# Kernel optimization log

Measured on AMD Instinct MI355X. Metric: run time of the kernel, lower is better.

## Reference

```python
import jax, jax.numpy as jnp
import numpy as np

DIM = 192; RES = (8, 56, 56); HEADS = 6; WS = (2, 7, 7); SS = (1, 3, 3)
B = 2
N_WIN_TOK = WS[0] * WS[1] * WS[2]  # 98


def _rel_pos_index():
    # 3D Swin relative position index, (N, N) int
    Wd, Wh, Ww = WS
    coords = np.stack(np.meshgrid(np.arange(Wd), np.arange(Wh), np.arange(Ww), indexing='ij'))
    coords = coords.reshape(3, -1)  # (3, N)
    rel = (coords[:, :, None] - coords[:, None, :]).transpose(1, 2, 0)  # (N, N, 3)
    rel[:, :, 0] += Wd - 1
    rel[:, :, 1] += Wh - 1
    rel[:, :, 2] += Ww - 1
    rel[:, :, 0] *= (2 * Wh - 1) * (2 * Ww - 1)
    rel[:, :, 1] *= (2 * Ww - 1)
    return rel.sum(-1)


def _attn_mask():
    # shifted-window mask (nW, N, N), 0 / -100
    D, H, W = RES; Wd, Wh, Ww = WS; sd, sh, sw = SS
    img = np.zeros((D, H, W))
    cnt = 0
    for ds in (slice(0, -Wd), slice(-Wd, -sd), slice(-sd, None)):
        for hs in (slice(0, -Wh), slice(-Wh, -sh), slice(-sh, None)):
            for ws_ in (slice(0, -Ww), slice(-Ww, -sw), slice(-sw, None)):
                img[ds, hs, ws_] = cnt
                cnt += 1
    win = img.reshape(D // Wd, Wd, H // Wh, Wh, W // Ww, Ww)
    win = win.transpose(0, 2, 4, 1, 3, 5).reshape(-1, N_WIN_TOK)  # (nW, N)
    diff = win[:, :, None] - win[:, None, :]
    return np.where(diff != 0, -100.0, 0.0).astype(np.float32)


_REL_IDX = _rel_pos_index()
_MASK = _attn_mask()


def _window_partition(x):
    # (B, D, H, W, C) -> (B*nW, N, C)
    Bb, D, H, W, C = x.shape
    Wd, Wh, Ww = WS
    x = x.reshape(Bb, D // Wd, Wd, H // Wh, Wh, W // Ww, Ww, C)
    x = x.transpose(0, 1, 3, 5, 2, 4, 6, 7)
    return x.reshape(-1, N_WIN_TOK, C)


def _window_reverse(x, Bb):
    # (B*nW, N, C) -> (B, D, H, W, C)
    D, H, W = RES; Wd, Wh, Ww = WS
    C = x.shape[-1]
    x = x.reshape(Bb, D // Wd, H // Wh, W // Ww, Wd, Wh, Ww, C)
    x = x.transpose(0, 1, 4, 2, 5, 3, 6, 7)
    return x.reshape(Bb, D, H, W, C)


def _layernorm(x, g, b, eps=1e-5):
    mu = jnp.mean(x, -1, keepdims=True)
    var = jnp.var(x, -1, keepdims=True)
    return (x - mu) * jax.lax.rsqrt(var + eps) * g + b


def setup_inputs() -> dict:
    key = jax.random.key(0)
    ks = jax.random.split(key, 8)
    L = RES[0] * RES[1] * RES[2]
    s = 0.02
    return {
        'x': jax.random.normal(ks[0], (B, L, DIM), jnp.float32),
        'norm1_g': jnp.ones((DIM,), jnp.float32),
        'norm1_b': jnp.zeros((DIM,), jnp.float32),
        'qkv_w': jax.random.normal(ks[1], (3 * DIM, DIM), jnp.float32) * s,
        'qkv_b': jax.random.normal(ks[2], (3 * DIM,), jnp.float32) * s,
        'rel_table': jax.random.normal(ks[3], ((2 * WS[0] - 1) * (2 * WS[1] - 1) * (2 * WS[2] - 1), HEADS), jnp.float32) * s,
        'norm2_g': jnp.ones((DIM,), jnp.float32),
        'norm2_b': jnp.zeros((DIM,), jnp.float32),
        'mlp_w1': jax.random.normal(ks[4], (4 * DIM, DIM), jnp.float32) * s,
        'mlp_b1': jax.random.normal(ks[5], (4 * DIM,), jnp.float32) * s,
        'mlp_w2': jax.random.normal(ks[6], (DIM, 4 * DIM), jnp.float32) * s,
        'mlp_b2': jax.random.normal(ks[7], (4 * DIM // 4,), jnp.float32) * s,
    }


def reference(x, norm1_g, norm1_b, qkv_w, qkv_b, rel_table, norm2_g, norm2_b, mlp_w1, mlp_b1, mlp_w2, mlp_b2):
    Bb, L, C = x.shape
    D, H, W = RES
    hd = C // HEADS
    scale = hd ** (-0.5)

    short_cut = x
    xn = _layernorm(x, norm1_g, norm1_b).reshape(Bb, D, H, W, C)
    xs = jnp.roll(xn, (-SS[0], -SS[1], -SS[2]), axis=(1, 2, 3))
    xw = _window_partition(xs)  # (Bn, N, C)
    Bn, N, _ = xw.shape

    # qkv grouping matches original: (nH hD qkv), qkv fastest axis
    qkv = (jnp.einsum('bnc,oc->bno', xw, qkv_w) + qkv_b).reshape(Bn, N, HEADS, hd, 3)
    q = qkv[..., 0].transpose(0, 2, 1, 3)  # (Bn, nH, N, hd)
    k = qkv[..., 1].transpose(0, 2, 1, 3)
    v = qkv[..., 2].transpose(0, 2, 1, 3)

    attn = jnp.einsum('bhnd,bhmd->bhnm', q, k) * scale
    bias = rel_table[jnp.asarray(_REL_IDX.reshape(-1))].reshape(N, N, HEADS)
    attn = attn + bias.transpose(2, 0, 1)[None]  # (Bn, nH, N, N)

    mask = jnp.asarray(_MASK)  # (nW, N, N)
    nW = mask.shape[0]
    attn = attn.reshape(Bb, nW, HEADS, N, N) + mask[None, :, None]
    attn = jax.nn.softmax(attn.reshape(Bn, HEADS, N, N), axis=-1)

    out = jnp.einsum('bhnm,bhmd->bhnd', attn, v)
    out = out.transpose(0, 2, 1, 3).reshape(Bn, N, C)

    xr = _window_reverse(out, Bb)
    x2 = jnp.roll(xr, (SS[0], SS[1], SS[2]), axis=(1, 2, 3)).reshape(Bb, L, C) + short_cut

    short_cut2 = x2
    h = _layernorm(x2, norm2_g, norm2_b)
    h = jax.nn.relu(jnp.einsum('blc,oc->blo', h, mlp_w1) + mlp_b1)
    h = jax.nn.relu(jnp.einsum('blo,co->blc', h, mlp_w2) + mlp_b2)
    return h + short_cut2
```

## Files before the change

### kernel.cpp

```cpp
#include <hip/hip_runtime.h>

typedef unsigned short u16;
typedef unsigned int   u32;
typedef __attribute__((ext_vector_type(4))) float f32x4;
typedef __attribute__((ext_vector_type(8))) short s16x8;
typedef __attribute__((ext_vector_type(4))) u32   u32x4;
typedef __attribute__((ext_vector_type(4))) u16   u16x4;

#define DEV static __device__ __forceinline__

DEV float bf2f(u16 a) { union { u32 u; float f; } x; x.u = ((u32)a) << 16; return x.f; }
DEV u16 f2bf(float f) {
  union { float f; u32 u; } x; x.f = f;
  u32 r = (x.u + 0x7FFFu + ((x.u >> 16) & 1u)) >> 16;
  return (u16)r;
}
DEV float wsum(float v) {
#pragma unroll
  for (int m = 32; m; m >>= 1) v += __shfl_xor(v, m, 64);
  return v;
}

DEV void gload16(const void* g, void* l) {
  __builtin_amdgcn_global_load_lds(
      (const __attribute__((address_space(1))) u32*)g,
      (__attribute__((address_space(3))) u32*)l, 16, 0, 0);
}

DEV const s16x8* frag(const u16* lds, int row, int s) {
  int sw = (s & ~7) | ((s & 7) ^ (row & 7));
  return reinterpret_cast<const s16x8*>(
      reinterpret_cast<const char*>(lds) + row * 384 + sw * 16);
}


__global__ __launch_bounds__(256) void k_prep(
    const float* __restrict__ qkvw, const float* __restrict__ qkvb,
    u16* __restrict__ qkvwb, float* __restrict__ pbias,
    const float* __restrict__ w1, u16* __restrict__ w1b,
    const float* __restrict__ relt, u16* __restrict__ biasT)
{
  int b = blockIdx.x, tid = threadIdx.x;
  if (b < 108) {
    const float sc = 0.17677669529663687f;
    int i = b * 256 + tid;
    if (i < 27648) {
      int np = i / 48, c = i - np * 48;
      int t = np / 192, rem = np - t * 192;
      int head = rem >> 5, dd = rem & 31;
      int o = head * 96 + dd * 3 + t;
      float s2 = (t == 0) ? sc : 1.f;
      f32x4 v = reinterpret_cast<const f32x4*>(qkvw)[o * 48 + c];
      u16x4 ov; ov[0] = f2bf(v[0] * s2); ov[1] = f2bf(v[1] * s2);
      ov[2] = f2bf(v[2] * s2); ov[3] = f2bf(v[3] * s2);
      reinterpret_cast<u16x4*>(qkvwb)[i] = ov;
    }
    if (i < 576) {
      int t = i / 192, rem = i - t * 192;
      int head = rem >> 5, dd = rem & 31;
      pbias[i] = qkvb[head * 96 + dd * 3 + t] * ((t == 0) ? sc : 1.f);
    }
  } else if (b < 252) {
    int i = (b - 108) * 256 + tid;
    if (i < 36864) {
      f32x4 v = reinterpret_cast<const f32x4*>(w1)[i];
      u16x4 o; o[0] = f2bf(v[0]); o[1] = f2bf(v[1]); o[2] = f2bf(v[2]); o[3] = f2bf(v[3]);
      reinterpret_cast<u16x4*>(w1b)[i] = o;
    }
  } else {
    int i = (b - 252) * 256 + tid;
    if (i >= 602112) return;
    int t = i % 112; int rem = i / 112;
    int j = rem % 112; rem /= 112;
    int h = rem % 6; int c = rem / 6;
    if (j >= 98) { biasT[i] = f2bf(-1e30f); return; }
    if (t >= 98) { biasT[i] = 0; return; }
    int td = t >= 49, tr = t - td * 49, th = tr / 7, tw = tr - th * 7;
    int jd = j >= 49, jr = j - jd * 49, jh = jr / 7, jw = jr - jh * 7;
    int lin_t = td * 169 + th * 13 + tw;
    int lin_j = jd * 169 + jh * 13 + jw;
    float bias = relt[(lin_t - lin_j + 253) * 6 + h];
    int cd = (c >> 2) & 1, ch = (c >> 1) & 1, cw = c & 1;
    int cnt_t = (cd ? (1 + td) : 0) * 9 + (ch ? (1 + (th >= 4)) : 0) * 3 + (cw ? (1 + (tw >= 4)) : 0);
    int cnt_j = (cd ? (1 + jd) : 0) * 9 + (ch ? (1 + (jh >= 4)) : 0) * 3 + (cw ? (1 + (jw >= 4)) : 0);
    if (cnt_t != cnt_j) bias -= 100.f;
    biasT[i] = f2bf(bias);
  }
}

__global__ __launch_bounds__(256) void k_wconv(const float* __restrict__ s, u16* __restrict__ d, int n4) {
  int i = blockIdx.x * 256 + threadIdx.x;
  if (i < n4) {
    f32x4 v = reinterpret_cast<const f32x4*>(s)[i];
    u16x4 o; o[0] = f2bf(v[0]); o[1] = f2bf(v[1]); o[2] = f2bf(v[2]); o[3] = f2bf(v[3]);
    reinterpret_cast<u16x4*>(d)[i] = o;
  }
}

__global__ __launch_bounds__(256) void k_ln1_win(
    const float* __restrict__ x, const float* __restrict__ g, const float* __restrict__ b,
    u16* __restrict__ xw)
{
  int row  = blockIdx.x * 4 + (threadIdx.x >> 6);
  int lane = threadIdx.x & 63;
  int win = row / 98, tok = row - win * 98;
  int bb = win >> 8, wrem = win & 255;
  int wd = wrem >> 6, wh = (wrem >> 3) & 7, ww = wrem & 7;
  int td = tok >= 49; int tr = tok - td * 49; int th = tr / 7, tw = tr - th * 7;
  int dsrc = (wd * 2 + td + 1) & 7;
  int hs = wh * 7 + th + 3; if (hs >= 56) hs -= 56;
  int wsc = ww * 7 + tw + 3; if (wsc >= 56) wsc -= 56;
  const float* xr = x + ((size_t)bb * 25088 + (size_t)dsrc * 3136 + hs * 56 + wsc) * 192;
  float v0 = xr[lane], v1 = xr[lane + 64], v2 = xr[lane + 128];
  float mu  = wsum(v0 + v1 + v2) * (1.f / 192.f);
  float sq  = wsum(v0 * v0 + v1 * v1 + v2 * v2) * (1.f / 192.f);
  float inv = rsqrtf(sq - mu * mu + 1e-5f);
  u16* orow = xw + (size_t)row * 192;
  orow[lane      ] = f2bf((v0 - mu) * inv * g[lane      ] + b[lane      ]);
  orow[lane + 64 ] = f2bf((v1 - mu) * inv * g[lane + 64 ] + b[lane + 64 ]);
  orow[lane + 128] = f2bf((v2 - mu) * inv * g[lane + 128] + b[lane + 128]);
}

__global__ __launch_bounds__(256) void k_merge_ln2(
    const float* __restrict__ x, const u16* __restrict__ ao,
    const float* __restrict__ g, const float* __restrict__ b,
    u16* __restrict__ x2b, u16* __restrict__ xn2)
{
  int m = blockIdx.x * 4 + (threadIdx.x >> 6);
  int lane = threadIdx.x & 63;
  int bb = m / 25088, l = m - bb * 25088;
  int d = l / 3136; int rem = l - d * 3136; int h = rem / 56, w = rem - h * 56;
  int dsh = (d + 7) & 7;
  int hsh = h - 3; if (hsh < 0) hsh += 56;
  int wsh = w - 3; if (wsh < 0) wsh += 56;
  int wd = dsh >> 1, td = dsh & 1;
  int wh = hsh / 7, th = hsh - wh * 7;
  int ww = wsh / 7, tw = wsh - ww * 7;
  int win = (bb << 8) + (wd << 6) + (wh << 3) + ww;
  int tok = td * 49 + th * 7 + tw;
  const u16* ar = ao + ((size_t)win * 98 + tok) * 192;
  const float* xr = x + (size_t)m * 192;
  float v0 = xr[lane      ] + bf2f(ar[lane      ]);
  float v1 = xr[lane + 64 ] + bf2f(ar[lane + 64 ]);
  float v2 = xr[lane + 128] + bf2f(ar[lane + 128]);
  u16* x2r = x2b + (size_t)m * 192;
  x2r[lane] = f2bf(v0); x2r[lane + 64] = f2bf(v1); x2r[lane + 128] = f2bf(v2);
  float mu  = wsum(v0 + v1 + v2) * (1.f / 192.f);
  float sq  = wsum(v0 * v0 + v1 * v1 + v2 * v2) * (1.f / 192.f);
  float inv = rsqrtf(sq - mu * mu + 1e-5f);
  u16* nr = xn2 + (size_t)m * 192;
  nr[lane      ] = f2bf((v0 - mu) * inv * g[lane      ] + b[lane      ]);
  nr[lane + 64 ] = f2bf((v1 - mu) * inv * g[lane + 64 ] + b[lane + 64 ]);
  nr[lane + 128] = f2bf((v2 - mu) * inv * g[lane + 128] + b[lane + 128]);
}

template<bool RELU, int NTOT>
__global__ __launch_bounds__(256) void k_gemm3(
    const u16* __restrict__ A, const u16* __restrict__ Wb, const float* __restrict__ bias,
    u16* __restrict__ C)
{
  constexpr int MG = 8;
  __shared__ u16 As[2][64 * 192];
  int bid = blockIdx.x;
  int nb = bid / 98, mg = bid - nb * 98;
  int n0 = nb * 96;
  int m_base = mg * (MG * 64);
  int tid = threadIdx.x, lane = tid & 63, wv = tid >> 6;
  int lr = lane & 15, lg = lane >> 4;
  int wm = wv >> 1, wn = wv & 1;

  auto stage = [&](int buf, int mt) {
    const char* gb = (const char*)(A + (size_t)(m_base + mt * 64) * 192);
    char* lb = (char*)As[buf] + wv * 6144;
#pragma unroll
    for (int c = 0; c < 6144; c += 1024) {
      int o = wv * 6144 + c + lane * 16;
      int row = (int)((u32)o / 384u);
      int slot = (o - row * 384) >> 4;
      int sw = (slot & ~7) | ((slot & 7) ^ (row & 7));
      gload16(gb + (size_t)row * 384 + sw * 16, lb + c);
    }
  };

  stage(0, 0);

  s16x8 wf[3][6];
  const u16* wbase = Wb + (size_t)(n0 + wn * 48 + lr) * 192 + lg * 8;
#pragma unroll
  for (int nf = 0; nf < 3; ++nf)
#pragma unroll
    for (int ks = 0; ks < 6; ++ks)
      wf[nf][ks] = *reinterpret_cast<const s16x8*>(wbase + (size_t)nf * 16 * 192 + ks * 32);
  float bs[3];
#pragma unroll
  for (int nf = 0; nf < 3; ++nf) bs[nf] = bias[n0 + wn * 48 + nf * 16 + lr];

  __syncthreads();
  for (int i = 0; i < MG; ++i) {
    int cur = i & 1;
    if (i + 1 < MG) stage(cur ^ 1, i + 1);
    f32x4 acc[2][3];
#pragma unroll
    for (int a = 0; a < 2; ++a)
#pragma unroll
      for (int nf = 0; nf < 3; ++nf) acc[a][nf] = {0.f, 0.f, 0.f, 0.f};
#pragma unroll
    for (int ks = 0; ks < 6; ++ks) {
      int s = ks * 4 + lg;
      s16x8 a0 = *frag(As[cur], wm * 32 + lr, s);
      s16x8 a1 = *frag(As[cur], wm * 32 + 16 + lr, s);
#pragma unroll
      for (int nf = 0; nf < 3; ++nf) {
        acc[0][nf] = __builtin_amdgcn_mfma_f32_16x16x32_bf16(a0, wf[nf][ks], acc[0][nf], 0, 0, 0);
        acc[1][nf] = __builtin_amdgcn_mfma_f32_16x16x32_bf16(a1, wf[nf][ks], acc[1][nf], 0, 0, 0);
      }
    }
    int m0 = m_base + i * 64;
#pragma unroll
    for (int mi = 0; mi < 2; ++mi)
#pragma unroll
      for (int nf = 0; nf < 3; ++nf)
#pragma unroll
        for (int r = 0; r < 4; ++r) {
          int m = m0 + wm * 32 + mi * 16 + lg * 4 + r;
          int n = n0 + wn * 48 + nf * 16 + lr;
          float val = acc[mi][nf][r] + bs[nf];
          if (RELU) val = fmaxf(val, 0.f);
          C[(size_t)m * NTOT + n] = f2bf(val);
        }
    __syncthreads();
  }
}

__global__ __launch_bounds__(512) void k_gemm2mlp2(
    const u16* __restrict__ A, const u16* __restrict__ Wb, const float* __restrict__ bias,
    const u16* __restrict__ x2b, float* __restrict__ of)
{
  constexpr int MB = 784;
  constexpr int KTOT = 768;
  __shared__ u16 As[64 * 192];
  __shared__ u16 Ws[96 * 192];
  int bid = blockIdx.x;
  int nb = bid / MB, mb = bid - nb * MB;
  int m0 = mb * 64, n0 = nb * 96;
  int tid = threadIdx.x, lane = tid & 63, wv = tid >> 6;
  int lr = lane & 15, lg = lane >> 4;
  int wm = wv >> 1, wn = wv & 1;

  f32x4 acc[3];
#pragma unroll
  for (int j = 0; j < 3; ++j) acc[j] = {0.f, 0.f, 0.f, 0.f};

  for (int kc = 0; kc < 4; ++kc) {
    if (kc) __syncthreads();
    if (wv < 4) {
      const char* gb = (const char*)(A + (size_t)m0 * KTOT + kc * 192);
      int base = wv * 6144;
#pragma unroll
      for (int c = 0; c < 6144; c += 1024) {
        int o = base + c + lane * 16;
        int row = (int)((u32)o / 384u);
        int slot = (o - row * 384) >> 4;
        int sw = (slot & ~7) | ((slot & 7) ^ (row & 7));
        gload16(gb + (size_t)row * (KTOT * 2) + sw * 16, (char*)As + base + c);
      }
    } else {
      const char* gb = (const char*)(Wb + (size_t)n0 * KTOT + kc * 192);
      int base = (wv - 4) * 9216;
#pragma unroll
      for (int c = 0; c < 9216; c += 1024) {
        int o = base + c + lane * 16;
        int row = (int)((u32)o / 384u);
        int slot = (o - row * 384) >> 4;
        int sw = (slot & ~7) | ((slot & 7) ^ (row & 7));
        gload16(gb + (size_t)row * (KTOT * 2) + sw * 16, (char*)Ws + base + c);
      }
    }
    __syncthreads();
#pragma unroll
    for (int ks = 0; ks < 6; ++ks) {
      int s = ks * 4 + lg;
      s16x8 a0 = *frag(As, wm * 16 + lr, s);
#pragma unroll
      for (int nf = 0; nf < 3; ++nf) {
        s16x8 bfr = *frag(Ws, wn * 48 + nf * 16 + lr, s);
        acc[nf] = __builtin_amdgcn_mfma_f32_16x16x32_bf16(a0, bfr, acc[nf], 0, 0, 0);
      }
    }
  }
#pragma unroll
  for (int nf = 0; nf < 3; ++nf)
#pragma unroll
    for (int r = 0; r < 4; ++r) {
      int m = m0 + wm * 16 + lg * 4 + r;
      int n = n0 + wn * 48 + nf * 16 + lr;
      size_t idx = (size_t)m * 192 + n;
      of[idx] = fmaxf(acc[nf][r] + bias[n], 0.f) + bf2f(x2b[idx]);
    }
}

__global__ __launch_bounds__(448, 2) void k_attn_mfma(
    const u16* __restrict__ qkvc, const u16* __restrict__ biasT, u16* __restrict__ ao)
{
  __shared__ u16 P[7][16 * 128];
  __shared__ u16 Vt[32 * 136];
  __shared__ u16 Ks[98 * 40];

  int bid = blockIdx.x;
  int win = bid / 6, head = bid - win * 6;
  int tid = threadIdx.x, lane = tid & 63, wv = tid >> 6;
  int lr = lane & 15, lg = lane >> 4;
  size_t rb = (size_t)(win * 98) * 576;
  const u16* qp0 = qkvc + rb + head * 32;
  const u16* kp0 = qkvc + rb + 192 + head * 32;
  const u16* vp0 = qkvc + rb + 384 + head * 32;

  int wrem = win & 255;
  int wd = wrem >> 6, wh = (wrem >> 3) & 7, ww = wrem & 7;
  int cls = ((wd == 3) ? 4 : 0) | ((wh == 7) ? 2 : 0) | ((ww == 7) ? 1 : 0);
  const u16* bT = biasT + (size_t)(cls * 6 + head) * 112 * 112;

  int qrow = wv * 16 + lr; if (qrow > 97) qrow = 97;
  s16x8 qf = *reinterpret_cast<const s16x8*>(qp0 + (size_t)qrow * 576 + lg * 8);
  u16x4 b4[7];
#pragma unroll
  for (int j = 0; j < 7; ++j) {
    int col = j * 16 + lr;
    b4[j] = *reinterpret_cast<const u16x4*>(bT + (size_t)col * 112 + wv * 16 + lg * 4);
  }

  for (int u = tid; u < 98 * 16; u += 448) {
    int tok = u >> 4, dp = (u & 15) * 2;
    u32 w = *reinterpret_cast<const u32*>(vp0 + (size_t)tok * 576 + dp);
    Vt[dp * 136 + tok]       = (u16)(w & 0xFFFFu);
    Vt[(dp + 1) * 136 + tok] = (u16)(w >> 16);
    u32 wk = *reinterpret_cast<const u32*>(kp0 + (size_t)tok * 576 + dp);
    *reinterpret_cast<u32*>(&Ks[tok * 40 + dp]) = wk;
  }
  for (int u = tid; u < 32 * 19; u += 448) {
    int d = u / 19, kslot = u - d * 19;
    *reinterpret_cast<u32*>(reinterpret_cast<char*>(Vt) + d * 272 + 196 + kslot * 4) = 0;
  }
  __syncthreads();

  f32x4 s[7];
  __builtin_amdgcn_s_setprio(1);
#pragma unroll
  for (int j = 0; j < 7; ++j) {
    int row = j * 16 + lr; if (row > 97) row = 97;
    s16x8 kfj = *reinterpret_cast<const s16x8*>(&Ks[row * 40 + lg * 8]);
    f32x4 c4;
#pragma unroll
    for (int r = 0; r < 4; ++r) c4[r] = bf2f(b4[j][r]);
    s[j] = __builtin_amdgcn_mfma_f32_16x16x32_bf16(qf, kfj, c4, 0, 0, 0);
  }
  __builtin_amdgcn_s_setprio(0);

  float sm[4] = {0.f, 0.f, 0.f, 0.f};
#pragma unroll
  for (int j = 0; j < 7; ++j)
#pragma unroll
    for (int r = 0; r < 4; ++r) {
      float p = __expf(s[j][r]);
      s[j][r] = p;
      sm[r] += p;
    }
#pragma unroll
  for (int m = 1; m < 16; m <<= 1)
#pragma unroll
    for (int r = 0; r < 4; ++r) sm[r] += __shfl_xor(sm[r], m, 64);
  float rinv[4];
#pragma unroll
  for (int r = 0; r < 4; ++r) rinv[r] = 1.f / sm[r];

#pragma unroll
  for (int j = 0; j < 7; ++j) {
    int col = j * 16 + lr;
    int slot = col >> 3, wi = col & 7;
#pragma unroll
    for (int r = 0; r < 4; ++r) {
      int lrow = lg * 4 + r;
      P[wv][lrow * 128 + (((slot ^ (lrow & 7)) << 3) | wi)] = f2bf(s[j][r]);
    }
  }
  if (lane < 32) {
    int lrow = lr;
    int slot = 14 + lg;
    u32x4 z4 = {0u, 0u, 0u, 0u};
    *reinterpret_cast<u32x4*>(&P[wv][lrow * 128 + ((slot ^ (lrow & 7)) << 3)]) = z4;
  }

  f32x4 o0 = {0.f, 0.f, 0.f, 0.f}, o1 = {0.f, 0.f, 0.f, 0.f};
  __builtin_amdgcn_s_setprio(1);
#pragma unroll
  for (int kc = 0; kc < 4; ++kc) {
    int slot = kc * 4 + lg;
    s16x8 pf = *reinterpret_cast<const s16x8*>(&P[wv][lr * 128 + ((slot ^ (lr & 7)) << 3)]);
    s16x8 vf0 = *reinterpret_cast<const s16x8*>(&Vt[lr * 136 + kc * 32 + lg * 8]);
    s16x8 vf1 = *reinterpret_cast<const s16x8*>(&Vt[(16 + lr) * 136 + kc * 32 + lg * 8]);
    o0 = __builtin_amdgcn_mfma_f32_16x16x32_bf16(pf, vf0, o0, 0, 0, 0);
    o1 = __builtin_amdgcn_mfma_f32_16x16x32_bf16(pf, vf1, o1, 0, 0, 0);
  }
  __builtin_amdgcn_s_setprio(0);
#pragma unroll
  for (int r = 0; r < 4; ++r) {
    int t = wv * 16 + lg * 4 + r;
    if (t < 98) {
      size_t ob = ((size_t)win * 98 + t) * 192 + head * 32;
      ao[ob + lr]      = f2bf(o0[r] * rinv[r]);
      ao[ob + 16 + lr] = f2bf(o1[r] * rinv[r]);
    }
  }
}

extern "C" void kernel_launch(void* const* d_in, const int* in_sizes, int n_in,
                              void* d_out, int out_size, void* d_ws, size_t ws_size,
                              hipStream_t stream) {
  (void)in_sizes; (void)n_in; (void)out_size; (void)ws_size;
  const float* x    = (const float*)d_in[0];
  const float* n1g  = (const float*)d_in[1];
  const float* n1b  = (const float*)d_in[2];
  const float* qkvw = (const float*)d_in[3];
  const float* qkvb = (const float*)d_in[4];
  const float* relt = (const float*)d_in[5];
  const float* n2g  = (const float*)d_in[6];
  const float* n2b  = (const float*)d_in[7];
  const float* w1   = (const float*)d_in[8];
  const float* b1   = (const float*)d_in[9];
  const float* w2   = (const float*)d_in[10];
  const float* b2   = (const float*)d_in[11];
  float* out = (float*)d_out;
  char* ws = (char*)d_ws;

  constexpr size_t SZB = 50176ull * 192 * 2;
  u16*  xw    = (u16*)(ws);
  u16*  qkvc  = (u16*)(ws + SZB);
  u16*  x2b   = (u16*)(ws + SZB);
  u16*  xn2   = (u16*)(ws + 3 * SZB);
  u16*  h1    = (u16*)(ws + 4 * SZB);
  u16*  ao    = xw;

  u16*   qkvwb = (u16*)out;
  u16*   w1b   = (u16*)((char*)out + 221184);
  float* pbias = (float*)((char*)out + 516096);
  u16*   biasT = (u16*)((char*)out + 520192);
  u16*   w2b   = (u16*)(ws + 3 * SZB);

  k_prep<<<2604, 256, 0, stream>>>(qkvw, qkvb, qkvwb, pbias, w1, w1b, relt, biasT);
  k_ln1_win<<<12544, 256, 0, stream>>>(x, n1g, n1b, xw);
  k_gemm3<false, 576><<<6 * 98, 256, 0, stream>>>(xw, qkvwb, pbias, qkvc);
  k_attn_mfma<<<3072, 448, 0, stream>>>(qkvc, biasT, ao);
  k_merge_ln2<<<12544, 256, 0, stream>>>(x, ao, n2g, n2b, x2b, xn2);
  k_gemm3<true, 768><<<8 * 98, 256, 0, stream>>>(xn2, w1b, b1, h1);
  k_wconv<<<144, 256, 0, stream>>>(w2, w2b, 147456 / 4);
  k_gemm2mlp2<<<784 * 2, 512, 0, stream>>>(h1, w2b, b2, x2b, out);
}
```

Baseline: 180.8 us.

## Merge prep/LN1 and w2 conversion into neighboring kernels, add XCD-aware block swizzle

Folds the LN1 window-partition kernel into the prep kernel and the w2 bf16 conversion into the MLP1 GEMM launch as extra blocks, cutting two kernel launches. It also remaps block indices so that consecutive logical tiles land on the same XCD, which is meant to improve L2 locality on the chiplet GPU. w2b now reuses the xw buffer, which is free once attention has consumed it. The catch is that the extra blocks share a launch with heavier GEMM blocks, and the swizzle reorders the schedule.

```diff
diff --git a/kernel.cpp b/kernel.cpp
--- a/kernel.cpp
+++ b/kernel.cpp
@@ -21,6 +21,12 @@
   return v;
 }
 
+DEV int xcd_swz(int bid, int nwg) {
+  int q = nwg >> 3, r = nwg & 7;
+  int xcd = bid & 7, idx = bid >> 3;
+  return (xcd < r ? xcd * (q + 1) : r * (q + 1) + (xcd - r) * q) + idx;
+}
+
 DEV void gload16(const void* g, void* l) {
   __builtin_amdgcn_global_load_lds(
       (const __attribute__((address_space(1))) u32*)g,
@@ -38,7 +44,9 @@
     const float* __restrict__ qkvw, const float* __restrict__ qkvb,
     u16* __restrict__ qkvwb, float* __restrict__ pbias,
     const float* __restrict__ w1, u16* __restrict__ w1b,
-    const float* __restrict__ relt, u16* __restrict__ biasT)
+    const float* __restrict__ relt, u16* __restrict__ biasT,
+    const float* __restrict__ x, const float* __restrict__ n1g,
+    const float* __restrict__ n1b, u16* __restrict__ xw)
 {
   int b = blockIdx.x, tid = threadIdx.x;
   if (b < 108) {
@@ -67,7 +75,7 @@
       u16x4 o; o[0] = f2bf(v[0]); o[1] = f2bf(v[1]); o[2] = f2bf(v[2]); o[3] = f2bf(v[3]);
       reinterpret_cast<u16x4*>(w1b)[i] = o;
     }
-  } else {
+  } else if (b < 2604) {
     int i = (b - 252) * 256 + tid;
     if (i >= 602112) return;
     int t = i % 112; int rem = i / 112;
@@ -85,40 +93,26 @@
     int cnt_j = (cd ? (1 + jd) : 0) * 9 + (ch ? (1 + (jh >= 4)) : 0) * 3 + (cw ? (1 + (jw >= 4)) : 0);
     if (cnt_t != cnt_j) bias -= 100.f;
     biasT[i] = f2bf(bias);
-  }
-}
-
-__global__ __launch_bounds__(256) void k_wconv(const float* __restrict__ s, u16* __restrict__ d, int n4) {
-  int i = blockIdx.x * 256 + threadIdx.x;
-  if (i < n4) {
-    f32x4 v = reinterpret_cast<const f32x4*>(s)[i];
-    u16x4 o; o[0] = f2bf(v[0]); o[1] = f2bf(v[1]); o[2] = f2bf(v[2]); o[3] = f2bf(v[3]);
-    reinterpret_cast<u16x4*>(d)[i] = o;
-  }
-}
-
-__global__ __launch_bounds__(256) void k_ln1_win(
-    const float* __restrict__ x, const float* __restrict__ g, const float* __restrict__ b,
-    u16* __restrict__ xw)
-{
-  int row  = blockIdx.x * 4 + (threadIdx.x >> 6);
-  int lane = threadIdx.x & 63;
-  int win = row / 98, tok = row - win * 98;
-  int bb = win >> 8, wrem = win & 255;
-  int wd = wrem >> 6, wh = (wrem >> 3) & 7, ww = wrem & 7;
-  int td = tok >= 49; int tr = tok - td * 49; int th = tr / 7, tw = tr - th * 7;
-  int dsrc = (wd * 2 + td + 1) & 7;
-  int hs = wh * 7 + th + 3; if (hs >= 56) hs -= 56;
-  int wsc = ww * 7 + tw + 3; if (wsc >= 56) wsc -= 56;
-  const float* xr = x + ((size_t)bb * 25088 + (size_t)dsrc * 3136 + hs * 56 + wsc) * 192;
-  float v0 = xr[lane], v1 = xr[lane + 64], v2 = xr[lane + 128];
-  float mu  = wsum(v0 + v1 + v2) * (1.f / 192.f);
-  float sq  = wsum(v0 * v0 + v1 * v1 + v2 * v2) * (1.f / 192.f);
-  float inv = rsqrtf(sq - mu * mu + 1e-5f);
-  u16* orow = xw + (size_t)row * 192;
-  orow[lane      ] = f2bf((v0 - mu) * inv * g[lane      ] + b[lane      ]);
-  orow[lane + 64 ] = f2bf((v1 - mu) * inv * g[lane + 64 ] + b[lane + 64 ]);
-  orow[lane + 128] = f2bf((v2 - mu) * inv * g[lane + 128] + b[lane + 128]);
+  } else {
+    int row  = (b - 2604) * 4 + (tid >> 6);
+    int lane = tid & 63;
+    int win = row / 98, tok = row - win * 98;
+    int bb = win >> 8, wrem = win & 255;
+    int wd = wrem >> 6, wh = (wrem >> 3) & 7, ww = wrem & 7;
+    int td = tok >= 49; int tr = tok - td * 49; int th = tr / 7, tw = tr - th * 7;
+    int dsrc = (wd * 2 + td + 1) & 7;
+    int hs = wh * 7 + th + 3; if (hs >= 56) hs -= 56;
+    int wsc = ww * 7 + tw + 3; if (wsc >= 56) wsc -= 56;
+    const float* xr = x + ((size_t)bb * 25088 + (size_t)dsrc * 3136 + hs * 56 + wsc) * 192;
+    float v0 = xr[lane], v1 = xr[lane + 64], v2 = xr[lane + 128];
+    float mu  = wsum(v0 + v1 + v2) * (1.f / 192.f);
+    float sq  = wsum(v0 * v0 + v1 * v1 + v2 * v2) * (1.f / 192.f);
+    float inv = rsqrtf(sq - mu * mu + 1e-5f);
+    u16* orow = xw + (size_t)row * 192;
+    orow[lane      ] = f2bf((v0 - mu) * inv * n1g[lane      ] + n1b[lane      ]);
+    orow[lane + 64 ] = f2bf((v1 - mu) * inv * n1g[lane + 64 ] + n1b[lane + 64 ]);
+    orow[lane + 128] = f2bf((v2 - mu) * inv * n1g[lane + 128] + n1b[lane + 128]);
+  }
 }
 
 __global__ __launch_bounds__(256) void k_merge_ln2(
@@ -157,11 +151,22 @@
 template<bool RELU, int NTOT>
 __global__ __launch_bounds__(256) void k_gemm3(
     const u16* __restrict__ A, const u16* __restrict__ Wb, const float* __restrict__ bias,
-    u16* __restrict__ C)
+    u16* __restrict__ C, const float* __restrict__ w2src, u16* __restrict__ w2dst)
 {
   constexpr int MG = 8;
+  constexpr int MAINW = (NTOT / 96) * 98;
   __shared__ u16 As[2][64 * 192];
   int bid = blockIdx.x;
+  if (RELU && bid >= MAINW) {
+    int i = (bid - MAINW) * 256 + threadIdx.x;
+    if (i < 36864) {
+      f32x4 v = reinterpret_cast<const f32x4*>(w2src)[i];
+      u16x4 o; o[0] = f2bf(v[0]); o[1] = f2bf(v[1]); o[2] = f2bf(v[2]); o[3] = f2bf(v[3]);
+      reinterpret_cast<u16x4*>(w2dst)[i] = o;
+    }
+    return;
+  }
+  bid = xcd_swz(bid, MAINW);
   int nb = bid / 98, mg = bid - nb * 98;
   int n0 = nb * 96;
   int m_base = mg * (MG * 64);
@@ -240,7 +245,7 @@
   constexpr int KTOT = 768;
   __shared__ u16 As[64 * 192];
   __shared__ u16 Ws[96 * 192];
-  int bid = blockIdx.x;
+  int bid = xcd_swz(blockIdx.x, 2 * MB);
   int nb = bid / MB, mb = bid - nb * MB;
   int m0 = mb * 64, n0 = nb * 96;
   int tid = threadIdx.x, lane = tid & 63, wv = tid >> 6;
@@ -306,7 +311,7 @@
   __shared__ u16 Vt[32 * 136];
   __shared__ u16 Ks[98 * 40];
 
-  int bid = blockIdx.x;
+  int bid = xcd_swz(blockIdx.x, 3072);
   int win = bid / 6, head = bid - win * 6;
   int tid = threadIdx.x, lane = tid & 63, wv = tid >> 6;
   int lr = lane & 15, lg = lane >> 4;
@@ -439,19 +444,18 @@
   u16*  xn2   = (u16*)(ws + 3 * SZB);
   u16*  h1    = (u16*)(ws + 4 * SZB);
   u16*  ao    = xw;
+  u16*  w2b   = xw;
 
   u16*   qkvwb = (u16*)out;
   u16*   w1b   = (u16*)((char*)out + 221184);
   float* pbias = (float*)((char*)out + 516096);
   u16*   biasT = (u16*)((char*)out + 520192);
-  u16*   w2b   = (u16*)(ws + 3 * SZB);
-
-  k_prep<<<2604, 256, 0, stream>>>(qkvw, qkvb, qkvwb, pbias, w1, w1b, relt, biasT);
-  k_ln1_win<<<12544, 256, 0, stream>>>(x, n1g, n1b, xw);
-  k_gemm3<false, 576><<<6 * 98, 256, 0, stream>>>(xw, qkvwb, pbias, qkvc);
+
+  k_prep<<<2604 + 12544, 256, 0, stream>>>(qkvw, qkvb, qkvwb, pbias, w1, w1b, relt, biasT,
+                                           x, n1g, n1b, xw);
+  k_gemm3<false, 576><<<6 * 98, 256, 0, stream>>>(xw, qkvwb, pbias, qkvc, nullptr, nullptr);
   k_attn_mfma<<<3072, 448, 0, stream>>>(qkvc, biasT, ao);
   k_merge_ln2<<<12544, 256, 0, stream>>>(x, ao, n2g, n2b, x2b, xn2);
-  k_gemm3<true, 768><<<8 * 98, 256, 0, stream>>>(xn2, w1b, b1, h1);
-  k_wconv<<<144, 256, 0, stream>>>(w2, w2b, 147456 / 4);
+  k_gemm3<true, 768><<<8 * 98 + 144, 256, 0, stream>>>(xn2, w1b, b1, h1, w2, w2b);
   k_gemm2mlp2<<<784 * 2, 512, 0, stream>>>(h1, w2b, b2, x2b, out);
 }
```

New measurement: 176.9 us. 1.02x faster.
